# Kernel optimization log

Hardware: AMD Instinct MI355X
Metric: run time of the kernel (lower is better)

The kernel has to match this reference:

```python
import jax, jax.numpy as jnp
import numpy as np

ALPHA = 0.2  # LeakyReLU negative slope


def setup_inputs() -> dict:
    key = jax.random.key(0)
    k1, k2, k3, k4 = jax.random.split(key, 4)
    B, N, IN_F, OUT_F = 8, 2048, 128, 64
    inputs = jax.random.normal(k1, (B, N, IN_F), dtype=jnp.float32)
    nodes_embedding = jax.random.normal(k2, (B, N, OUT_F), dtype=jnp.float32)
    # xavier-uniform-like init (gain 1.414)
    limW = 1.414 * np.sqrt(6.0 / (IN_F + OUT_F))
    W = jax.random.uniform(k3, (IN_F, OUT_F), dtype=jnp.float32, minval=-limW, maxval=limW)
    lima = 1.414 * np.sqrt(6.0 / (4 * OUT_F + 1))
    a = jax.random.uniform(k4, (4 * OUT_F, 1), dtype=jnp.float32, minval=-lima, maxval=lima)
    return {"inputs": inputs, "nodes_embedding": nodes_embedding, "W": W, "a": a}


def reference(inputs, nodes_embedding, W, a):
    # x_w: [B,N,F]
    x_w = jnp.matmul(inputs, W)
    # h: [B,N,2F]
    h = jnp.concatenate([nodes_embedding, x_w], axis=2)
    twoF = h.shape[-1]
    # Separable form of concat-based attention: a_input[b,i,j] = [h_i, h_j],
    # so a_input @ a = (h_i . a1) + (h_j . a2). Avoids the O(B*N^2*4F) tensor.
    a1 = a[:twoF, 0]  # [2F]
    a2 = a[twoF:, 0]  # [2F]
    s1 = jnp.einsum('bnf,f->bn', h, a1)  # [B,N]
    s2 = jnp.einsum('bnf,f->bn', h, a2)  # [B,N]
    e = jax.nn.leaky_relu(s1[:, :, None] + s2[:, None, :], negative_slope=ALPHA)  # [B,N,N]
    attention = jax.nn.softmax(e, axis=2)  # softmax over j
    # dropout: eval mode (training=False) -> identity
    h_prime = jnp.matmul(attention, x_w)  # [B,N,F]
    return (jax.nn.relu(h_prime), attention)
```

## Files before the change

### kernel.cpp

```cpp
#include <hip/hip_runtime.h>

#define ALPHA 0.2f
#define B_    8
#define N_    2048
#define INF_  128
#define OUTF_ 64
#define LOG2E 1.4426950408889634f

typedef __attribute__((ext_vector_type(8))) short short8;
typedef __attribute__((ext_vector_type(4))) float f32x4;

__device__ __forceinline__ unsigned short f2bf(float f) {
    unsigned int x = __float_as_uint(f);
    return (unsigned short)((x + 0x7fffu + ((x >> 16) & 1u)) >> 16);
}

__global__ __launch_bounds__(256) void prep_kernel(
    const float* __restrict__ inp,
    const float* __restrict__ nodes,
    const float* __restrict__ Wm,
    const float* __restrict__ av,
    unsigned short* __restrict__ xwT,
    float* __restrict__ s1_out,
    float* __restrict__ s2_out)
{
    __shared__ float w_lds[INF_ * OUTF_];
    __shared__ __align__(16) unsigned short t_lds[64 * 40];
    const int tid  = threadIdx.x;
    const int wave = tid >> 6, lane = tid & 63;
    const int r0   = blockIdx.x * 32;

    {
        const float4* Wv = (const float4*)Wm;
        float4* wd = (float4*)w_lds;
        #pragma unroll
        for (int q = 0; q < 8; q++) wd[tid + q * 256] = Wv[tid + q * 256];
    }
    __syncthreads();

    const int wv = __builtin_amdgcn_readfirstlane(wave);
    const float* __restrict__ rbase = inp + (size_t)(r0 + wv * 8) * INF_;

    float acc0[8] = {0.f,0.f,0.f,0.f,0.f,0.f,0.f,0.f};
    float acc1[8] = {0.f,0.f,0.f,0.f,0.f,0.f,0.f,0.f};
    #pragma unroll 4
    for (int k = 0; k < INF_; k += 2) {
        const float w0 = w_lds[k * OUTF_ + lane];
        const float w1 = w_lds[(k + 1) * OUTF_ + lane];
        #pragma unroll
        for (int rr = 0; rr < 8; rr++) {
            acc0[rr] += rbase[rr * INF_ + k]     * w0;
            acc1[rr] += rbase[rr * INF_ + k + 1] * w1;
        }
    }
    float acc[8];
    #pragma unroll
    for (int rr = 0; rr < 8; rr++) acc[rr] = acc0[rr] + acc1[rr];

    const float a1n = av[lane];
    const float a1x = av[64 + lane];
    const float a2n = av[128 + lane];
    const float a2x = av[192 + lane];

    #pragma unroll
    for (int rr = 0; rr < 8; rr++) {
        const int row = r0 + wv * 8 + rr;
        float nf = nodes[(size_t)row * OUTF_ + lane];
        float p1 = nf * a1n + acc[rr] * a1x;
        float p2 = nf * a2n + acc[rr] * a2x;
        #pragma unroll
        for (int off = 32; off; off >>= 1) {
            p1 += __shfl_down(p1, off);
            p2 += __shfl_down(p2, off);
        }
        if (lane == 0) { s1_out[row] = p1; s2_out[row] = p2; }
        t_lds[lane * 40 + wv * 8 + rr] = f2bf(acc[rr]);
    }
    __syncthreads();

    {
        const int f = tid >> 2, g = tid & 3;
        const int b = r0 >> 11, rb = r0 & (N_ - 1);
        *(uint4*)(xwT + ((size_t)b * OUTF_ + f) * N_ + rb + g * 8) =
            *(const uint4*)&t_lds[f * 40 + g * 8];
    }
}

__global__ __launch_bounds__(512, 2) void attn_kernel(
    const unsigned short* __restrict__ xwT,
    const float* __restrict__ s1g,
    const float* __restrict__ s2g,
    float* __restrict__ out_h,
    float* __restrict__ out_att)
{
    __shared__ float s2L[N_];
    __shared__ float s2A[N_];
    __shared__ float s1_lds[64];
    __shared__ float c1_lds[64];
    __shared__ float c2_lds[64];
    __shared__ float redmax[8];
    __shared__ f32x4 redacc[4][64][4];

    const int tid  = threadIdx.x;
    const int wave = tid >> 6, lane = tid & 63;
    const int b  = blockIdx.x & 7;
    const int i0 = (blockIdx.x >> 3) << 6;

    {
        float4 v = *(const float4*)(s2g + b * N_ + tid * 4);
        float lm = fmaxf(fmaxf(v.x, v.y), fmaxf(v.z, v.w));
        *(float4*)&s2L[tid * 4] = make_float4(v.x * LOG2E, v.y * LOG2E,
                                              v.z * LOG2E, v.w * LOG2E);
        *(float4*)&s2A[tid * 4] = make_float4(v.x * (ALPHA * LOG2E), v.y * (ALPHA * LOG2E),
                                              v.z * (ALPHA * LOG2E), v.w * (ALPHA * LOG2E));
        #pragma unroll
        for (int off = 32; off; off >>= 1) lm = fmaxf(lm, __shfl_xor(lm, off));
        if (lane == 0) redmax[wave] = lm;
    }
    if (tid < 64) s1_lds[tid] = s1g[b * N_ + i0 + tid];
    __syncthreads();

    float s2max = redmax[0];
    #pragma unroll
    for (int w = 1; w < 8; w++) s2max = fmaxf(s2max, redmax[w]);

    {
        const int row = tid >> 3, jo = tid & 7;
        const float s1v = s1_lds[row];
        const float vm  = s1v + s2max;
        const float mL  = (vm > 0.f ? vm : ALPHA * vm) * LOG2E;
        const float d1  = s1v * LOG2E - mL;
        const float d2  = s1v * (ALPHA * LOG2E) - mL;
        float l = 0.f;
        for (int j = jo * 4; j < N_; j += 32) {
            float4 xl = *(const float4*)&s2L[j];
            float4 xa = *(const float4*)&s2A[j];
            l += __builtin_amdgcn_exp2f(fmaxf(d1 + xl.x, d2 + xa.x));
            l += __builtin_amdgcn_exp2f(fmaxf(d1 + xl.y, d2 + xa.y));
            l += __builtin_amdgcn_exp2f(fmaxf(d1 + xl.z, d2 + xa.z));
            l += __builtin_amdgcn_exp2f(fmaxf(d1 + xl.w, d2 + xa.w));
        }
        l += __shfl_xor(l, 1);
        l += __shfl_xor(l, 2);
        l += __shfl_xor(l, 4);
        if (jo == 0) {
            const float lg = __builtin_amdgcn_logf(l);
            c1_lds[row] = d1 - lg;
            c2_lds[row] = d2 - lg;
        }
    }
    __syncthreads();

    const int row16 = lane & 15;
    const int quad  = lane >> 4;
    const int wsub  = wave & 3;
    const int jh    = wave >> 2;
    const int irow  = wsub * 16 + row16;
    const float c1  = c1_lds[irow];
    const float c2  = c2_lds[irow];
    const int jb    = jh * 1024;

    const unsigned short* bptr[4];
    #pragma unroll
    for (int g = 0; g < 4; g++)
        bptr[g] = xwT + ((size_t)b * OUTF_ + g * 16 + row16) * N_ + jb + quad * 8;

    float* attp = out_att + ((size_t)(b * N_ + i0 + irow)) * N_ + jb + quad * 8;
    const float* pL = s2L + jb + quad * 8;
    const float* pA = s2A + jb + quad * 8;

    f32x4 acc0 = {0.f,0.f,0.f,0.f}, acc1 = {0.f,0.f,0.f,0.f};
    f32x4 acc2 = {0.f,0.f,0.f,0.f}, acc3 = {0.f,0.f,0.f,0.f};

    uint4 bnext[4];
    #pragma unroll
    for (int g = 0; g < 4; g++) bnext[g] = *(const uint4*)bptr[g];

    for (int jt = 0; jt < 1024; jt += 32) {
        uint4 bc0 = bnext[0], bc1 = bnext[1], bc2 = bnext[2], bc3 = bnext[3];
        const int jn = (jt + 32) & 1023;
        #pragma unroll
        for (int g = 0; g < 4; g++) bnext[g] = *(const uint4*)(bptr[g] + jn);

        float4 sa = *(const float4*)(pL + jt);
        float4 sb = *(const float4*)(pL + jt + 4);
        float4 ta = *(const float4*)(pA + jt);
        float4 tb = *(const float4*)(pA + jt + 4);
        float av8[8];
        av8[0] = __builtin_amdgcn_exp2f(fmaxf(c1 + sa.x, c2 + ta.x));
        av8[1] = __builtin_amdgcn_exp2f(fmaxf(c1 + sa.y, c2 + ta.y));
        av8[2] = __builtin_amdgcn_exp2f(fmaxf(c1 + sa.z, c2 + ta.z));
        av8[3] = __builtin_amdgcn_exp2f(fmaxf(c1 + sa.w, c2 + ta.w));
        av8[4] = __builtin_amdgcn_exp2f(fmaxf(c1 + sb.x, c2 + tb.x));
        av8[5] = __builtin_amdgcn_exp2f(fmaxf(c1 + sb.y, c2 + tb.y));
        av8[6] = __builtin_amdgcn_exp2f(fmaxf(c1 + sb.z, c2 + tb.z));
        av8[7] = __builtin_amdgcn_exp2f(fmaxf(c1 + sb.w, c2 + tb.w));

        f32x4 o0 = {av8[0], av8[1], av8[2], av8[3]};
        f32x4 o1 = {av8[4], av8[5], av8[6], av8[7]};
        __builtin_nontemporal_store(o0, (f32x4*)(attp + jt));
        __builtin_nontemporal_store(o1, (f32x4*)(attp + jt + 4));

        short8 a8;
        #pragma unroll
        for (int jj = 0; jj < 8; jj++) a8[jj] = (short)f2bf(av8[jj]);

        acc0 = __builtin_amdgcn_mfma_f32_16x16x32_bf16(a8, *(short8*)&bc0, acc0, 0, 0, 0);
        acc1 = __builtin_amdgcn_mfma_f32_16x16x32_bf16(a8, *(short8*)&bc1, acc1, 0, 0, 0);
        acc2 = __builtin_amdgcn_mfma_f32_16x16x32_bf16(a8, *(short8*)&bc2, acc2, 0, 0, 0);
        acc3 = __builtin_amdgcn_mfma_f32_16x16x32_bf16(a8, *(short8*)&bc3, acc3, 0, 0, 0);
    }

    if (wave >= 4) {
        redacc[wsub][lane][0] = acc0;
        redacc[wsub][lane][1] = acc1;
        redacc[wsub][lane][2] = acc2;
        redacc[wsub][lane][3] = acc3;
    }
    __syncthreads();
    if (wave < 4) {
        acc0 += redacc[wsub][lane][0];
        acc1 += redacc[wsub][lane][1];
        acc2 += redacc[wsub][lane][2];
        acc3 += redacc[wsub][lane][3];
        const size_t hb = ((size_t)(b * N_) + i0 + wsub * 16) * OUTF_;
        #pragma unroll
        for (int r = 0; r < 4; r++) {
            const size_t ro = hb + (size_t)(quad * 4 + r) * OUTF_ + row16;
            __builtin_nontemporal_store(fmaxf(acc0[r], 0.f), out_h + ro);
            __builtin_nontemporal_store(fmaxf(acc1[r], 0.f), out_h + ro + 16);
            __builtin_nontemporal_store(fmaxf(acc2[r], 0.f), out_h + ro + 32);
            __builtin_nontemporal_store(fmaxf(acc3[r], 0.f), out_h + ro + 48);
        }
    }
}

extern "C" void kernel_launch(void* const* d_in, const int* in_sizes, int n_in,
                              void* d_out, int out_size, void* d_ws, size_t ws_size,
                              hipStream_t stream) {
    const float* inp   = (const float*)d_in[0];
    const float* nodes = (const float*)d_in[1];
    const float* Wm    = (const float*)d_in[2];
    const float* av    = (const float*)d_in[3];

    float* out_h   = (float*)d_out;
    float* out_att = out_h + (size_t)B_ * N_ * OUTF_;

    unsigned short* xwT = (unsigned short*)d_ws;
    float* s1_ws = (float*)((char*)d_ws + (size_t)B_ * OUTF_ * N_ * sizeof(unsigned short));
    float* s2_ws = s1_ws + (size_t)B_ * N_;

    prep_kernel<<<(B_ * N_) / 32, 256, 0, stream>>>(inp, nodes, Wm, av,
                                                    xwT, s1_ws, s2_ws);
    attn_kernel<<<256, 512, 0, stream>>>(xwT, s1_ws, s2_ws, out_h, out_att);
}
```

Measured before the change: 226.2 us.

## Stage input rows in LDS for prep and use plain stores for outputs

The prep kernel now handles 16 rows per block instead of 32. It stages the input rows into LDS with coalesced float4 loads instead of reading global memory with strided scalar accesses, and uses narrower transpose writes. Separately, the attention kernel replaces its nontemporal stores for the attention matrix and output with ordinary stores. The prep change targets uncoalesced global reads. The store change trades streaming hints for normal cache behaviour on a 134MB output write, which may hurt or help.

```diff
diff --git a/kernel.cpp b/kernel.cpp
--- a/kernel.cpp
+++ b/kernel.cpp
@@ -25,37 +25,34 @@
     float* __restrict__ s2_out)
 {
     __shared__ float w_lds[INF_ * OUTF_];
-    __shared__ __align__(16) unsigned short t_lds[64 * 40];
+    __shared__ float in_lds[16 * INF_];
+    __shared__ __align__(16) unsigned short t_lds[64 * 16];
     const int tid  = threadIdx.x;
     const int wave = tid >> 6, lane = tid & 63;
-    const int r0   = blockIdx.x * 32;
+    const int r0   = blockIdx.x * 16;
 
     {
         const float4* Wv = (const float4*)Wm;
         float4* wd = (float4*)w_lds;
         #pragma unroll
         for (int q = 0; q < 8; q++) wd[tid + q * 256] = Wv[tid + q * 256];
-    }
-    __syncthreads();
-
-    const int wv = __builtin_amdgcn_readfirstlane(wave);
-    const float* __restrict__ rbase = inp + (size_t)(r0 + wv * 8) * INF_;
-
-    float acc0[8] = {0.f,0.f,0.f,0.f,0.f,0.f,0.f,0.f};
-    float acc1[8] = {0.f,0.f,0.f,0.f,0.f,0.f,0.f,0.f};
+        const float4* Iv = (const float4*)(inp + (size_t)r0 * INF_);
+        float4* id4 = (float4*)in_lds;
+        id4[tid]       = Iv[tid];
+        id4[tid + 256] = Iv[tid + 256];
+    }
+    __syncthreads();
+
+    float acc[4] = {0.f, 0.f, 0.f, 0.f};
+    const float* inw = &in_lds[(wave * 4) * INF_];
     #pragma unroll 4
-    for (int k = 0; k < INF_; k += 2) {
-        const float w0 = w_lds[k * OUTF_ + lane];
-        const float w1 = w_lds[(k + 1) * OUTF_ + lane];
-        #pragma unroll
-        for (int rr = 0; rr < 8; rr++) {
-            acc0[rr] += rbase[rr * INF_ + k]     * w0;
-            acc1[rr] += rbase[rr * INF_ + k + 1] * w1;
-        }
-    }
-    float acc[8];
-    #pragma unroll
-    for (int rr = 0; rr < 8; rr++) acc[rr] = acc0[rr] + acc1[rr];
+    for (int k = 0; k < INF_; k++) {
+        float wv = w_lds[k * OUTF_ + lane];
+        acc[0] += inw[k]            * wv;
+        acc[1] += inw[INF_ + k]     * wv;
+        acc[2] += inw[2 * INF_ + k] * wv;
+        acc[3] += inw[3 * INF_ + k] * wv;
+    }
 
     const float a1n = av[lane];
     const float a1x = av[64 + lane];
@@ -63,8 +60,8 @@
     const float a2x = av[192 + lane];
 
     #pragma unroll
-    for (int rr = 0; rr < 8; rr++) {
-        const int row = r0 + wv * 8 + rr;
+    for (int rr = 0; rr < 4; rr++) {
+        const int row = r0 + wave * 4 + rr;
         float nf = nodes[(size_t)row * OUTF_ + lane];
         float p1 = nf * a1n + acc[rr] * a1x;
         float p2 = nf * a2n + acc[rr] * a2x;
@@ -74,15 +71,15 @@
             p2 += __shfl_down(p2, off);
         }
         if (lane == 0) { s1_out[row] = p1; s2_out[row] = p2; }
-        t_lds[lane * 40 + wv * 8 + rr] = f2bf(acc[rr]);
-    }
-    __syncthreads();
-
-    {
-        const int f = tid >> 2, g = tid & 3;
-        const int b = r0 >> 11, rb = r0 & (N_ - 1);
-        *(uint4*)(xwT + ((size_t)b * OUTF_ + f) * N_ + rb + g * 8) =
-            *(const uint4*)&t_lds[f * 40 + g * 8];
+        t_lds[lane * 16 + wave * 4 + rr] = f2bf(acc[rr]);
+    }
+    __syncthreads();
+
+    {
+        const int n  = tid >> 2, c0 = (tid & 3) * 4;
+        const int b  = r0 >> 11, rb = r0 & (N_ - 1);
+        *(uint2*)(xwT + ((size_t)b * OUTF_ + n) * N_ + rb + c0) =
+            *(const uint2*)&t_lds[n * 16 + c0];
     }
 }
 
@@ -196,10 +193,8 @@
         av8[6] = __builtin_amdgcn_exp2f(fmaxf(c1 + sb.z, c2 + tb.z));
         av8[7] = __builtin_amdgcn_exp2f(fmaxf(c1 + sb.w, c2 + tb.w));
 
-        f32x4 o0 = {av8[0], av8[1], av8[2], av8[3]};
-        f32x4 o1 = {av8[4], av8[5], av8[6], av8[7]};
-        __builtin_nontemporal_store(o0, (f32x4*)(attp + jt));
-        __builtin_nontemporal_store(o1, (f32x4*)(attp + jt + 4));
+        *(float4*)(attp + jt)     = make_float4(av8[0], av8[1], av8[2], av8[3]);
+        *(float4*)(attp + jt + 4) = make_float4(av8[4], av8[5], av8[6], av8[7]);
 
         short8 a8;
         #pragma unroll
@@ -227,10 +222,10 @@
         #pragma unroll
         for (int r = 0; r < 4; r++) {
             const size_t ro = hb + (size_t)(quad * 4 + r) * OUTF_ + row16;
-            __builtin_nontemporal_store(fmaxf(acc0[r], 0.f), out_h + ro);
-            __builtin_nontemporal_store(fmaxf(acc1[r], 0.f), out_h + ro + 16);
-            __builtin_nontemporal_store(fmaxf(acc2[r], 0.f), out_h + ro + 32);
-            __builtin_nontemporal_store(fmaxf(acc3[r], 0.f), out_h + ro + 48);
+            out_h[ro]      = fmaxf(acc0[r], 0.f);
+            out_h[ro + 16] = fmaxf(acc1[r], 0.f);
+            out_h[ro + 32] = fmaxf(acc2[r], 0.f);
+            out_h[ro + 48] = fmaxf(acc3[r], 0.f);
         }
     }
 }
@@ -250,7 +245,7 @@
     float* s1_ws = (float*)((char*)d_ws + (size_t)B_ * OUTF_ * N_ * sizeof(unsigned short));
     float* s2_ws = s1_ws + (size_t)B_ * N_;
 
-    prep_kernel<<<(B_ * N_) / 32, 256, 0, stream>>>(inp, nodes, Wm, av,
+    prep_kernel<<<(B_ * N_) / 16, 256, 0, stream>>>(inp, nodes, Wm, av,
                                                     xwT, s1_ws, s2_ws);
     attn_kernel<<<256, 512, 0, stream>>>(xwT, s1_ws, s2_ws, out_h, out_att);
 }
```

Result: faster. 187.4 us, median of 2 (-17.2%).
